# Kernel tuning notes

Hardware: AMD Instinct MI355X
Metric: run time of the kernel (lower is better)

Reference implementation:

```python
import jax, jax.numpy as jnp
import numpy as np

LATENT = 128
DISC = 64
RNN = 512
CODE = 512
INPUT = 2


def _lstm_cell(x, h, c, Wih, Whh, bih, bhh):
    # PyTorch LSTMCell: gate order (i, f, g, o)
    gates = x @ Wih.T + h @ Whh.T + bih + bhh
    i, f, g, o = jnp.split(gates, 4, axis=-1)
    c_new = jax.nn.sigmoid(f) * c + jax.nn.sigmoid(i) * jnp.tanh(g)
    h_new = jax.nn.sigmoid(o) * jnp.tanh(c_new)
    return h_new, c_new


def setup_inputs() -> dict:
    key = jax.random.key(0)
    ks = jax.random.split(key, 12)
    B = 4096
    s = lambda *sh: 1.0 / np.sqrt(sh[-1])
    inp = {
        'latent': jax.random.normal(ks[0], (B, LATENT), dtype=jnp.float32),
        'W_unpack': jax.random.normal(ks[1], (CODE, LATENT + INPUT), dtype=jnp.float32) * s(CODE, LATENT + INPUT),
        'b_unpack': jnp.zeros((CODE,), dtype=jnp.float32),
        'Wih0': jax.random.normal(ks[2], (4 * RNN, CODE), dtype=jnp.float32) * s(4 * RNN, CODE),
        'Whh0': jax.random.normal(ks[3], (4 * RNN, RNN), dtype=jnp.float32) * s(4 * RNN, RNN),
        'bih0': jnp.zeros((4 * RNN,), dtype=jnp.float32),
        'bhh0': jnp.zeros((4 * RNN,), dtype=jnp.float32),
        'Wih1': jax.random.normal(ks[4], (4 * RNN, RNN), dtype=jnp.float32) * s(4 * RNN, RNN),
        'Whh1': jax.random.normal(ks[5], (4 * RNN, RNN), dtype=jnp.float32) * s(4 * RNN, RNN),
        'bih1': jnp.zeros((4 * RNN,), dtype=jnp.float32),
        'bhh1': jnp.zeros((4 * RNN,), dtype=jnp.float32),
        'W_angle': jax.random.normal(ks[6], (DISC, RNN), dtype=jnp.float32) * s(DISC, RNN),
        'b_angle': jnp.zeros((DISC,), dtype=jnp.float32),
        'num_segments': 64,
    }
    return inp


def reference(latent, W_unpack, b_unpack, Wih0, Whh0, bih0, bhh0,
              Wih1, Whh1, bih1, bhh1, W_angle, b_angle, num_segments):
    B = latent.shape[0]
    space = jnp.linspace(-1.0, 1.0, DISC, dtype=latent.dtype)  # [DISC]
    # fixed gumbel noise for all steps: [S, B, DISC]
    u = jax.random.uniform(jax.random.key(42), (num_segments, B, DISC),
                           dtype=latent.dtype, minval=1e-8, maxval=1.0)
    gumbels = -jnp.log(-jnp.log(u))

    def step(carry, g):
        prev, h0, c0, h1, c1 = carry
        x = jnp.tanh(jnp.concatenate([latent, prev], axis=-1) @ W_unpack.T + b_unpack)
        h0, c0 = _lstm_cell(x, h0, c0, Wih0, Whh0, bih0, bhh0)
        h1, c1 = _lstm_cell(h0, h1, c1, Wih1, Whh1, bih1, bhh1)
        logits = h1 @ W_angle.T + b_angle
        # gumbel-softmax, tau=1 (torch default), hard=True with straight-through
        y_soft = jax.nn.softmax(logits + g, axis=-1)
        y_hard = jax.nn.one_hot(jnp.argmax(y_soft, axis=-1), DISC, dtype=y_soft.dtype)
        y = y_soft + jax.lax.stop_gradient(y_hard - y_soft)
        angles = jnp.sum(y * space, axis=-1, keepdims=True)  # [B,1]
        seg = jnp.concatenate([angles, jnp.zeros_like(angles)], axis=-1)  # [B,2]
        return (seg, h0, c0, h1, c1), seg

    z = jnp.zeros((B, RNN), dtype=latent.dtype)
    init = (jnp.zeros((B, INPUT), dtype=latent.dtype), z, z, z, z)
    _, segs = jax.lax.scan(step, init, gumbels)  # [S, B, 2]
    return jnp.transpose(segs, (1, 0, 2))  # [B, S, 2]
```

## Files before the change

kernel.cpp:

```cpp
#include <hip/hip_runtime.h>
#include <cstdint>

#define BATCH 4096
#define LATENT 128
#define RNN 512
#define CODE 512
#define DISC 64
#define NSEG 64
#define UNPACK_COLS 130

__device__ __forceinline__ uint32_t rotl32(uint32_t x, uint32_t r) {
  return (x << r) | (x >> (32u - r));
}

__device__ __forceinline__ uint32_t threefry_bits(uint32_t n) {
  const uint32_t k0 = 0u, k1 = 42u;
  const uint32_t ks2 = k0 ^ k1 ^ 0x1BD11BDAu;
  uint32_t x0 = 0u, x1 = n;
  x0 += k0; x1 += k1;
#define TF_ROUND(r) { x0 += x1; x1 = rotl32(x1, r); x1 ^= x0; }
  TF_ROUND(13) TF_ROUND(15) TF_ROUND(26) TF_ROUND(6)
  x0 += k1;  x1 += ks2 + 1u;
  TF_ROUND(17) TF_ROUND(29) TF_ROUND(16) TF_ROUND(24)
  x0 += ks2; x1 += k0 + 2u;
  TF_ROUND(13) TF_ROUND(15) TF_ROUND(26) TF_ROUND(6)
  x0 += k0;  x1 += k1 + 3u;
  TF_ROUND(17) TF_ROUND(29) TF_ROUND(16) TF_ROUND(24)
  x0 += k1;  x1 += ks2 + 4u;
  TF_ROUND(13) TF_ROUND(15) TF_ROUND(26) TF_ROUND(6)
  x0 += ks2; x1 += k0 + 5u;
#undef TF_ROUND
  return x0 ^ x1;
}

__device__ __forceinline__ float sigmoidf_(float v) {
  return 1.0f / (1.0f + expf(-v));
}

__global__ __launch_bounds__(256) void base_kernel(
    const float* __restrict__ latent, const float* __restrict__ Wu,
    const float* __restrict__ bu, float* __restrict__ base) {
  __shared__ float lrow[LATENT];
  const int b = blockIdx.x;
  if (threadIdx.x < LATENT) lrow[threadIdx.x] = latent[b * LATENT + threadIdx.x];
  __syncthreads();
  for (int n = threadIdx.x; n < CODE; n += 256) {
    const float* wr = Wu + (size_t)n * UNPACK_COLS;
    float acc = 0.f;
#pragma unroll 8
    for (int k = 0; k < LATENT; ++k) acc += lrow[k] * wr[k];
    base[(size_t)b * CODE + n] = acc + bu[n];
  }
}

__global__ __launch_bounds__(256) void x_kernel(
    const float* __restrict__ base, const float* __restrict__ angle,
    const float* __restrict__ Wu, float* __restrict__ xo) {
  const int idx = blockIdx.x * 256 + threadIdx.x;
  const int b = idx >> 9;
  const int n = idx & 511;
  xo[idx] = tanhf(base[idx] + angle[b] * Wu[(size_t)n * UNPACK_COLS + 128]);
}

#define BM 128
#define BN 128
#define BK 16

__global__ __launch_bounds__(256) void gemm_lstm(
    const float* __restrict__ A1, const float* __restrict__ W1,
    const float* __restrict__ A2, const float* __restrict__ W2,
    const float* __restrict__ b1, const float* __restrict__ b2,
    float* __restrict__ c_io, float* __restrict__ h_out) {
  const int K = RNN;
  __shared__ __align__(16) float As[BK][BM];
  __shared__ __align__(16) float Ws[BK][BN];
  const int tid = threadIdx.x;
  const int tx = tid & 15, ty = tid >> 4;
  const int bx = blockIdx.x;
  const int rowBase = blockIdx.y * BM;
  const int lrow = tid >> 2;
  const int lk = (tid & 3) * 4;
  const int swz = (tid & 3) << 3;

  float acc[8][8];
#pragma unroll
  for (int i = 0; i < 8; ++i)
#pragma unroll
    for (int j = 0; j < 8; ++j) acc[i][j] = 0.f;

  for (int seg = 0; seg < 2; ++seg) {
    const float* __restrict__ A = seg ? A2 : A1;
    const float* __restrict__ W = seg ? W2 : W1;
    for (int k0 = 0; k0 < K; k0 += BK) {
      __syncthreads();
#pragma unroll
      for (int r = 0; r < 2; ++r) {
        const int rr = lrow + r * 64;
        const int cc = rr ^ swz;
        const float4 va = *(const float4*)&A[(size_t)(rowBase + rr) * K + k0 + lk];
        As[lk + 0][cc] = va.x; As[lk + 1][cc] = va.y;
        As[lk + 2][cc] = va.z; As[lk + 3][cc] = va.w;
        const int wn = ((rr >> 5) * RNN) + (bx << 5) + (rr & 31);
        const float4 vw = *(const float4*)&W[(size_t)wn * K + k0 + lk];
        Ws[lk + 0][cc] = vw.x; Ws[lk + 1][cc] = vw.y;
        Ws[lk + 2][cc] = vw.z; Ws[lk + 3][cc] = vw.w;
      }
      __syncthreads();
#pragma unroll
      for (int kk = 0; kk < BK; ++kk) {
        const int swk = (kk & 12) << 1;
        const float4 a0 = *(const float4*)&As[kk][(ty * 4) ^ swk];
        const float4 a1 = *(const float4*)&As[kk][(64 + ty * 4) ^ swk];
        const float4 w0 = *(const float4*)&Ws[kk][(tx * 4) ^ swk];
        const float4 w1 = *(const float4*)&Ws[kk][(64 + tx * 4) ^ swk];
        const float av[8] = {a0.x, a0.y, a0.z, a0.w, a1.x, a1.y, a1.z, a1.w};
        const float wv[8] = {w0.x, w0.y, w0.z, w0.w, w1.x, w1.y, w1.z, w1.w};
#pragma unroll
        for (int i = 0; i < 8; ++i)
#pragma unroll
          for (int j = 0; j < 8; ++j) acc[i][j] += av[i] * wv[j];
      }
    }
  }

  const int myjl = (tx & 7) * 4;
  const int jbase = (bx << 5) + myjl;
  const int g0 = (tx < 8) ? 0 : 1;
  const int g1 = g0 + 2;
  float bs0[4], bs1[4];
#pragma unroll
  for (int j = 0; j < 4; ++j) {
    bs0[j] = b1[g0 * RNN + jbase + j] + b2[g0 * RNN + jbase + j];
    bs1[j] = b1[g1 * RNN + jbase + j] + b2[g1 * RNN + jbase + j];
  }
  const bool low = (tx < 8);
#pragma unroll
  for (int i = 0; i < 8; ++i) {
    float v0[4], v1[4], p0[4], p1[4];
#pragma unroll
    for (int j = 0; j < 4; ++j) {
      v0[j] = acc[i][j] + bs0[j];
      v1[j] = acc[i][4 + j] + bs1[j];
      p0[j] = __shfl_xor(v0[j], 8);
      p1[j] = __shfl_xor(v1[j], 8);
    }
    const bool mine = low ? (i < 4) : (i >= 4);
    if (mine) {
      const int row = rowBase + (low ? (ty * 4 + i) : (64 + ty * 4 + (i - 4)));
      const size_t off = (size_t)row * RNN + jbase;
      const float4 cold = *(const float4*)&c_io[off];
      const float co[4] = {cold.x, cold.y, cold.z, cold.w};
      float cn[4], hn[4];
#pragma unroll
      for (int j = 0; j < 4; ++j) {
        const float fi = low ? v0[j] : p0[j];
        const float fg = low ? v1[j] : p1[j];
        const float ff = low ? p0[j] : v0[j];
        const float fo = low ? p1[j] : v1[j];
        const float c2 = sigmoidf_(ff) * co[j] + sigmoidf_(fi) * tanhf(fg);
        cn[j] = c2;
        hn[j] = sigmoidf_(fo) * tanhf(c2);
      }
      *(float4*)&c_io[off] = make_float4(cn[0], cn[1], cn[2], cn[3]);
      *(float4*)&h_out[off] = make_float4(hn[0], hn[1], hn[2], hn[3]);
    }
  }
}

__global__ __launch_bounds__(64) void head_kernel(
    const float* __restrict__ h1, const float* __restrict__ Wang,
    const float* __restrict__ bang, float* __restrict__ angle,
    float* __restrict__ out, int s) {
  const int b = blockIdx.x;
  const int d = threadIdx.x;
  const float4* hr = (const float4*)(h1 + (size_t)b * RNN);
  const float4* wr = (const float4*)(Wang + (size_t)d * RNN);
  float acc = 0.f;
#pragma unroll 16
  for (int k = 0; k < RNN / 4; ++k) {
    float4 a = hr[k], w = wr[k];
    acc += a.x * w.x; acc += a.y * w.y; acc += a.z * w.z; acc += a.w * w.w;
  }
  float z = acc + bang[d];
  const uint32_t n = ((uint32_t)s * BATCH + (uint32_t)b) * DISC + (uint32_t)d;
  const uint32_t bits = threefry_bits(n);
  const float f = __uint_as_float((bits >> 9) | 0x3f800000u) - 1.0f;
  const float u = fmaxf(1e-8f, f + 1e-8f);
  const float gum = -logf(-logf(u));
  z += gum;
  float m = z;
#pragma unroll
  for (int off = 32; off; off >>= 1) m = fmaxf(m, __shfl_xor(m, off));
  const float e = expf(z - m);
  float ssum = e;
#pragma unroll
  for (int off = 32; off; off >>= 1) ssum += __shfl_xor(ssum, off);
  const float y = e / ssum;
  float ymax = y;
#pragma unroll
  for (int off = 32; off; off >>= 1) ymax = fmaxf(ymax, __shfl_xor(ymax, off));
  const unsigned long long mask = __ballot(y == ymax);
  const int k = __ffsll(mask) - 1;
  if (d == 0) {
    const float sp = -1.0f + (2.0f / 63.0f) * (float)k;
    angle[b] = sp;
    out[((size_t)b * NSEG + s) * 2 + 0] = sp;
    out[((size_t)b * NSEG + s) * 2 + 1] = 0.0f;
  }
}

extern "C" void kernel_launch(void* const* d_in, const int* in_sizes, int n_in,
                              void* d_out, int out_size, void* d_ws, size_t ws_size,
                              hipStream_t stream) {
  const float* latent   = (const float*)d_in[0];
  const float* W_unpack = (const float*)d_in[1];
  const float* b_unpack = (const float*)d_in[2];
  const float* Wih0     = (const float*)d_in[3];
  const float* Whh0     = (const float*)d_in[4];
  const float* bih0     = (const float*)d_in[5];
  const float* bhh0     = (const float*)d_in[6];
  const float* Wih1     = (const float*)d_in[7];
  const float* Whh1     = (const float*)d_in[8];
  const float* bih1     = (const float*)d_in[9];
  const float* bhh1     = (const float*)d_in[10];
  const float* W_angle  = (const float*)d_in[11];
  const float* b_angle  = (const float*)d_in[12];
  float* out = (float*)d_out;

  const size_t HC = (size_t)BATCH * RNN;
  float* ws    = (float*)d_ws;
  float* h0a   = ws;
  float* h1a   = h0a + HC;
  float* c0    = h1a + HC;
  float* c1    = c0 + HC;
  float* angle = c1 + HC;
  float* h0b   = angle + BATCH;
  float* h1b   = h0b + HC;
  float* x     = h1b + HC;
  float* base  = x + (size_t)BATCH * CODE;

  hipMemsetAsync(ws, 0, (4 * HC + BATCH) * sizeof(float), stream);

  base_kernel<<<BATCH, 256, 0, stream>>>(latent, W_unpack, b_unpack, base);

  dim3 ggrid(16, 32);
  for (int s = 0; s < NSEG; ++s) {
    const int p = s & 1;
    float* h0p = p ? h0b : h0a; float* h0n = p ? h0a : h0b;
    float* h1p = p ? h1b : h1a; float* h1n = p ? h1a : h1b;
    x_kernel<<<(BATCH * CODE) / 256, 256, 0, stream>>>(base, angle, W_unpack, x);
    gemm_lstm<<<ggrid, 256, 0, stream>>>(x, Wih0, h0p, Whh0, bih0, bhh0, c0, h0n);
    gemm_lstm<<<ggrid, 256, 0, stream>>>(h0n, Wih1, h1p, Whh1, bih1, bhh1, c1, h1n);
    head_kernel<<<BATCH, 64, 0, stream>>>(h1n, W_angle, b_angle, angle, out, s);
  }
}
```

Before: 33.79 ms.

## Prefetch GEMM tiles into registers with BK=32 and stage head weights in LDS

The LSTM GEMM now uses a K tile of 32 and keeps the next tile's global loads in flight in registers while the current tile is computed from shared memory. This hides global load latency and halves the number of barrier pairs, with a new XOR swizzle sized for the wider tile. The head kernel now handles 16 batch rows per 256-thread block and loads W_angle once into 128KB of swizzled LDS, instead of each 64-thread block reading the whole matrix from global memory. The costs are higher register pressure in the GEMM and lower occupancy in the head kernel because of the large LDS footprint.

```diff
diff --git a/kernel.cpp b/kernel.cpp
--- a/kernel.cpp
+++ b/kernel.cpp
@@ -64,7 +64,8 @@
 
 #define BM 128
 #define BN 128
-#define BK 16
+#define BK 32
+#define KSTEPS 32
 
 __global__ __launch_bounds__(256) void gemm_lstm(
     const float* __restrict__ A1, const float* __restrict__ W1,
@@ -79,8 +80,8 @@
   const int bx = blockIdx.x;
   const int rowBase = blockIdx.y * BM;
   const int lrow = tid >> 2;
-  const int lk = (tid & 3) * 4;
-  const int swz = (tid & 3) << 3;
+  const int q = tid & 3;
+  const int lk = q * 4;
 
   float acc[8][8];
 #pragma unroll
@@ -88,40 +89,68 @@
 #pragma unroll
     for (int j = 0; j < 8; ++j) acc[i][j] = 0.f;
 
-  for (int seg = 0; seg < 2; ++seg) {
-    const float* __restrict__ A = seg ? A2 : A1;
-    const float* __restrict__ W = seg ? W2 : W1;
-    for (int k0 = 0; k0 < K; k0 += BK) {
-      __syncthreads();
-#pragma unroll
-      for (int r = 0; r < 2; ++r) {
-        const int rr = lrow + r * 64;
-        const int cc = rr ^ swz;
-        const float4 va = *(const float4*)&A[(size_t)(rowBase + rr) * K + k0 + lk];
-        As[lk + 0][cc] = va.x; As[lk + 1][cc] = va.y;
-        As[lk + 2][cc] = va.z; As[lk + 3][cc] = va.w;
-        const int wn = ((rr >> 5) * RNN) + (bx << 5) + (rr & 31);
-        const float4 vw = *(const float4*)&W[(size_t)wn * K + k0 + lk];
-        Ws[lk + 0][cc] = vw.x; Ws[lk + 1][cc] = vw.y;
-        Ws[lk + 2][cc] = vw.z; Ws[lk + 3][cc] = vw.w;
+  float4 ra[2][2], rw[2][2];
+
+  int wn[2];
+#pragma unroll
+  for (int r = 0; r < 2; ++r) {
+    const int rr = lrow + r * 64;
+    wn[r] = ((rr >> 5) * RNN) + (bx << 5) + (rr & 31);
+  }
+
+#define ISSUE_LOADS(step)                                                      \
+  {                                                                            \
+    const int seg_ = (step) >> 4;                                              \
+    const int k0_ = ((step) & 15) * BK;                                        \
+    const float* __restrict__ A_ = seg_ ? A2 : A1;                             \
+    const float* __restrict__ W_ = seg_ ? W2 : W1;                             \
+    _Pragma("unroll") for (int r = 0; r < 2; ++r) {                            \
+      const int rr_ = lrow + r * 64;                                           \
+      _Pragma("unroll") for (int kh = 0; kh < 2; ++kh) {                       \
+        ra[r][kh] = *(const float4*)&A_[(size_t)(rowBase + rr_) * K + k0_ +    \
+                                        kh * 16 + lk];                         \
+        rw[r][kh] = *(const float4*)&W_[(size_t)wn[r] * K + k0_ + kh * 16 +    \
+                                        lk];                                   \
+      }                                                                        \
+    }                                                                          \
+  }
+
+  ISSUE_LOADS(0)
+
+  for (int step = 0; step < KSTEPS; ++step) {
+    __syncthreads();
+#pragma unroll
+    for (int r = 0; r < 2; ++r) {
+      const int rr = lrow + r * 64;
+#pragma unroll
+      for (int kh = 0; kh < 2; ++kh) {
+        const int kq = q + kh * 4;
+        const int cc = rr ^ (kq << 3);
+        const int kb = kh * 16 + lk;
+        As[kb + 0][cc] = ra[r][kh].x; As[kb + 1][cc] = ra[r][kh].y;
+        As[kb + 2][cc] = ra[r][kh].z; As[kb + 3][cc] = ra[r][kh].w;
+        Ws[kb + 0][cc] = rw[r][kh].x; Ws[kb + 1][cc] = rw[r][kh].y;
+        Ws[kb + 2][cc] = rw[r][kh].z; Ws[kb + 3][cc] = rw[r][kh].w;
       }
-      __syncthreads();
-#pragma unroll
-      for (int kk = 0; kk < BK; ++kk) {
-        const int swk = (kk & 12) << 1;
-        const float4 a0 = *(const float4*)&As[kk][(ty * 4) ^ swk];
-        const float4 a1 = *(const float4*)&As[kk][(64 + ty * 4) ^ swk];
-        const float4 w0 = *(const float4*)&Ws[kk][(tx * 4) ^ swk];
-        const float4 w1 = *(const float4*)&Ws[kk][(64 + tx * 4) ^ swk];
-        const float av[8] = {a0.x, a0.y, a0.z, a0.w, a1.x, a1.y, a1.z, a1.w};
-        const float wv[8] = {w0.x, w0.y, w0.z, w0.w, w1.x, w1.y, w1.z, w1.w};
-#pragma unroll
-        for (int i = 0; i < 8; ++i)
-#pragma unroll
-          for (int j = 0; j < 8; ++j) acc[i][j] += av[i] * wv[j];
-      }
-    }
-  }
+    }
+    __syncthreads();
+    if (step + 1 < KSTEPS) ISSUE_LOADS(step + 1)
+#pragma unroll
+    for (int kk = 0; kk < BK; ++kk) {
+      const int swk = ((kk >> 2) & 7) << 3;
+      const float4 a0 = *(const float4*)&As[kk][(ty * 4) ^ swk];
+      const float4 a1 = *(const float4*)&As[kk][(64 + ty * 4) ^ swk];
+      const float4 w0 = *(const float4*)&Ws[kk][(tx * 4) ^ swk];
+      const float4 w1 = *(const float4*)&Ws[kk][(64 + tx * 4) ^ swk];
+      const float av[8] = {a0.x, a0.y, a0.z, a0.w, a1.x, a1.y, a1.z, a1.w};
+      const float wv[8] = {w0.x, w0.y, w0.z, w0.w, w1.x, w1.y, w1.z, w1.w};
+#pragma unroll
+      for (int i = 0; i < 8; ++i)
+#pragma unroll
+        for (int j = 0; j < 8; ++j) acc[i][j] += av[i] * wv[j];
+    }
+  }
+#undef ISSUE_LOADS
 
   const int myjl = (tx & 7) * 4;
   const int jbase = (bx << 5) + myjl;
@@ -167,45 +196,62 @@
   }
 }
 
-__global__ __launch_bounds__(64) void head_kernel(
+#define HROWS 16
+
+__global__ __launch_bounds__(256) void head_kernel(
     const float* __restrict__ h1, const float* __restrict__ Wang,
     const float* __restrict__ bang, float* __restrict__ angle,
     float* __restrict__ out, int s) {
-  const int b = blockIdx.x;
-  const int d = threadIdx.x;
-  const float4* hr = (const float4*)(h1 + (size_t)b * RNN);
-  const float4* wr = (const float4*)(Wang + (size_t)d * RNN);
-  float acc = 0.f;
+  __shared__ __align__(16) float4 Wl[DISC * 128];
+  const int tid = threadIdx.x;
+  for (int u = tid; u < DISC * 128; u += 256) {
+    const int d = u >> 7, k4 = u & 127;
+    Wl[(d << 7) | (k4 ^ (d & 7))] =
+        *(const float4*)&Wang[((size_t)d << 9) + (k4 << 2)];
+  }
+  __syncthreads();
+  const int wave = tid >> 6;
+  const int d = tid & 63;
+  const int dsw = d & 7;
+  const float bd = bang[d];
+  const int rowBase = blockIdx.x * HROWS + wave * 4;
+#pragma unroll 1
+  for (int rr = 0; rr < 4; ++rr) {
+    const int b = rowBase + rr;
+    const float4* __restrict__ hr = (const float4*)(h1 + ((size_t)b << 9));
+    float acc = 0.f;
 #pragma unroll 16
-  for (int k = 0; k < RNN / 4; ++k) {
-    float4 a = hr[k], w = wr[k];
-    acc += a.x * w.x; acc += a.y * w.y; acc += a.z * w.z; acc += a.w * w.w;
-  }
-  float z = acc + bang[d];
-  const uint32_t n = ((uint32_t)s * BATCH + (uint32_t)b) * DISC + (uint32_t)d;
-  const uint32_t bits = threefry_bits(n);
-  const float f = __uint_as_float((bits >> 9) | 0x3f800000u) - 1.0f;
-  const float u = fmaxf(1e-8f, f + 1e-8f);
-  const float gum = -logf(-logf(u));
-  z += gum;
-  float m = z;
-#pragma unroll
-  for (int off = 32; off; off >>= 1) m = fmaxf(m, __shfl_xor(m, off));
-  const float e = expf(z - m);
-  float ssum = e;
-#pragma unroll
-  for (int off = 32; off; off >>= 1) ssum += __shfl_xor(ssum, off);
-  const float y = e / ssum;
-  float ymax = y;
-#pragma unroll
-  for (int off = 32; off; off >>= 1) ymax = fmaxf(ymax, __shfl_xor(ymax, off));
-  const unsigned long long mask = __ballot(y == ymax);
-  const int k = __ffsll(mask) - 1;
-  if (d == 0) {
-    const float sp = -1.0f + (2.0f / 63.0f) * (float)k;
-    angle[b] = sp;
-    out[((size_t)b * NSEG + s) * 2 + 0] = sp;
-    out[((size_t)b * NSEG + s) * 2 + 1] = 0.0f;
+    for (int k4 = 0; k4 < 128; ++k4) {
+      const float4 a = hr[k4];
+      const float4 w = Wl[(d << 7) | (k4 ^ dsw)];
+      acc += a.x * w.x; acc += a.y * w.y; acc += a.z * w.z; acc += a.w * w.w;
+    }
+    float z = acc + bd;
+    const uint32_t n = ((uint32_t)s * BATCH + (uint32_t)b) * DISC + (uint32_t)d;
+    const uint32_t bits = threefry_bits(n);
+    const float f = __uint_as_float((bits >> 9) | 0x3f800000u) - 1.0f;
+    const float u = fmaxf(1e-8f, f + 1e-8f);
+    const float gum = -logf(-logf(u));
+    z += gum;
+    float m = z;
+#pragma unroll
+    for (int off = 32; off; off >>= 1) m = fmaxf(m, __shfl_xor(m, off));
+    const float e = expf(z - m);
+    float ssum = e;
+#pragma unroll
+    for (int off = 32; off; off >>= 1) ssum += __shfl_xor(ssum, off);
+    const float y = e / ssum;
+    float ymax = y;
+#pragma unroll
+    for (int off = 32; off; off >>= 1) ymax = fmaxf(ymax, __shfl_xor(ymax, off));
+    const unsigned long long mask = __ballot(y == ymax);
+    const int k = __ffsll(mask) - 1;
+    if (d == 0) {
+      const float sp = -1.0f + (2.0f / 63.0f) * (float)k;
+      angle[b] = sp;
+      out[((size_t)b * NSEG + s) * 2 + 0] = sp;
+      out[((size_t)b * NSEG + s) * 2 + 1] = 0.0f;
+    }
   }
 }
 
@@ -251,6 +297,6 @@
     x_kernel<<<(BATCH * CODE) / 256, 256, 0, stream>>>(base, angle, W_unpack, x);
     gemm_lstm<<<ggrid, 256, 0, stream>>>(x, Wih0, h0p, Whh0, bih0, bhh0, c0, h0n);
     gemm_lstm<<<ggrid, 256, 0, stream>>>(h0n, Wih1, h1p, Whh1, bih1, bhh1, c1, h1n);
-    head_kernel<<<BATCH, 64, 0, stream>>>(h1n, W_angle, b_angle, angle, out, s);
-  }
-}
+    head_kernel<<<BATCH / HROWS, 256, 0, stream>>>(h1n, W_angle, b_angle, angle, out, s);
+  }
+}
```

After: 45.69 ms. 35.2% more time.

## Restructure LSTM GEMM to 64x512 tiles with register-prefetched weights and direct A loads

Applied to the files above, without the earlier changes.

Replaces the 128x128 shared-memory tiled LSTM gate GEMM with 512-thread blocks that each cover 64 batch rows by 512 gate columns. Only the weight tile is staged in LDS, and the next K-slice is prefetched into registers while the current one is computed. Each wave reads its 8 A rows straight from global memory as float4. The block index is remapped so neighbouring blocks share weight or A tiles. This aims to raise reuse of each weight slice and overlap global loads with FMA work. The cost is heavy reliance on cache for the A-operand loads and higher register pressure under launch_bounds(512,2).

```diff
diff --git a/kernel.cpp b/kernel.cpp
--- a/kernel.cpp
+++ b/kernel.cpp
@@ -62,25 +62,26 @@
   xo[idx] = tanhf(base[idx] + angle[b] * Wu[(size_t)n * UNPACK_COLS + 128]);
 }
 
-#define BM 128
-#define BN 128
-#define BK 16
-
-__global__ __launch_bounds__(256) void gemm_lstm(
+#define BMW 64
+#define KSTEP 16
+
+__global__ __launch_bounds__(512, 2) void gemm_lstm(
     const float* __restrict__ A1, const float* __restrict__ W1,
     const float* __restrict__ A2, const float* __restrict__ W2,
     const float* __restrict__ b1, const float* __restrict__ b2,
     float* __restrict__ c_io, float* __restrict__ h_out) {
-  const int K = RNN;
-  __shared__ __align__(16) float As[BK][BM];
-  __shared__ __align__(16) float Ws[BK][BN];
+  __shared__ __align__(16) float Ws[KSTEP][512];
   const int tid = threadIdx.x;
-  const int tx = tid & 15, ty = tid >> 4;
-  const int bx = blockIdx.x;
-  const int rowBase = blockIdx.y * BM;
-  const int lrow = tid >> 2;
-  const int lk = (tid & 3) * 4;
-  const int swz = (tid & 3) << 3;
+  const int lane = tid & 63;
+  const int wv = tid >> 6;
+  const int d = blockIdx.x;
+  const int bx = (d & 7) >> 1;
+  const int by = ((d >> 3) << 1) | (d & 1);
+  const int rowBase = by * BMW;
+
+  const int wn = ((tid >> 7) * RNN) + (bx << 7) + (tid & 127);
+  const float* __restrict__ wrow1 = W1 + (size_t)wn * RNN;
+  const float* __restrict__ wrow2 = W2 + (size_t)wn * RNN;
 
   float acc[8][8];
 #pragma unroll
@@ -90,73 +91,91 @@
 
   for (int seg = 0; seg < 2; ++seg) {
     const float* __restrict__ A = seg ? A2 : A1;
-    const float* __restrict__ W = seg ? W2 : W1;
-    for (int k0 = 0; k0 < K; k0 += BK) {
+    const float* __restrict__ wrow = seg ? wrow2 : wrow1;
+    float4 st[4];
+#pragma unroll
+    for (int q = 0; q < 4; ++q) st[q] = *(const float4*)&wrow[q * 4];
+
+    for (int k0 = 0; k0 < RNN; k0 += KSTEP) {
       __syncthreads();
 #pragma unroll
-      for (int r = 0; r < 2; ++r) {
-        const int rr = lrow + r * 64;
-        const int cc = rr ^ swz;
-        const float4 va = *(const float4*)&A[(size_t)(rowBase + rr) * K + k0 + lk];
-        As[lk + 0][cc] = va.x; As[lk + 1][cc] = va.y;
-        As[lk + 2][cc] = va.z; As[lk + 3][cc] = va.w;
-        const int wn = ((rr >> 5) * RNN) + (bx << 5) + (rr & 31);
-        const float4 vw = *(const float4*)&W[(size_t)wn * K + k0 + lk];
-        Ws[lk + 0][cc] = vw.x; Ws[lk + 1][cc] = vw.y;
-        Ws[lk + 2][cc] = vw.z; Ws[lk + 3][cc] = vw.w;
+      for (int q = 0; q < 4; ++q) {
+        Ws[q * 4 + 0][tid] = st[q].x;
+        Ws[q * 4 + 1][tid] = st[q].y;
+        Ws[q * 4 + 2][tid] = st[q].z;
+        Ws[q * 4 + 3][tid] = st[q].w;
       }
       __syncthreads();
-#pragma unroll
-      for (int kk = 0; kk < BK; ++kk) {
-        const int swk = (kk & 12) << 1;
-        const float4 a0 = *(const float4*)&As[kk][(ty * 4) ^ swk];
-        const float4 a1 = *(const float4*)&As[kk][(64 + ty * 4) ^ swk];
-        const float4 w0 = *(const float4*)&Ws[kk][(tx * 4) ^ swk];
-        const float4 w1 = *(const float4*)&Ws[kk][(64 + tx * 4) ^ swk];
-        const float av[8] = {a0.x, a0.y, a0.z, a0.w, a1.x, a1.y, a1.z, a1.w};
-        const float wv[8] = {w0.x, w0.y, w0.z, w0.w, w1.x, w1.y, w1.z, w1.w};
+      if (k0 + KSTEP < RNN) {
+#pragma unroll
+        for (int q = 0; q < 4; ++q)
+          st[q] = *(const float4*)&wrow[k0 + KSTEP + q * 4];
+      }
+      const float* __restrict__ abase = A + (size_t)(rowBase + wv * 8) * RNN + k0;
+#pragma unroll
+      for (int c4 = 0; c4 < 4; ++c4) {
+        float4 af[8];
 #pragma unroll
         for (int i = 0; i < 8; ++i)
-#pragma unroll
-          for (int j = 0; j < 8; ++j) acc[i][j] += av[i] * wv[j];
+          af[i] = *(const float4*)&abase[(size_t)i * RNN + c4 * 4];
+        float4 wfA[4], wfB[4];
+#pragma unroll
+        for (int kk = 0; kk < 4; ++kk) {
+          wfA[kk] = *(const float4*)&Ws[c4 * 4 + kk][4 * lane];
+          wfB[kk] = *(const float4*)&Ws[c4 * 4 + kk][256 + 4 * lane];
+        }
+#pragma unroll
+        for (int kk = 0; kk < 4; ++kk) {
+#pragma unroll
+          for (int i = 0; i < 8; ++i) {
+            const float a = ((const float*)&af[i])[kk];
+            acc[i][0] += a * wfA[kk].x;
+            acc[i][1] += a * wfA[kk].y;
+            acc[i][2] += a * wfA[kk].z;
+            acc[i][3] += a * wfA[kk].w;
+            acc[i][4] += a * wfB[kk].x;
+            acc[i][5] += a * wfB[kk].y;
+            acc[i][6] += a * wfB[kk].z;
+            acc[i][7] += a * wfB[kk].w;
+          }
+        }
       }
     }
   }
 
-  const int myjl = (tx & 7) * 4;
-  const int jbase = (bx << 5) + myjl;
-  const int g0 = (tx < 8) ? 0 : 1;
-  const int g1 = g0 + 2;
-  float bs0[4], bs1[4];
+  const int col0 = (bx << 7) + 4 * (lane & 31);
+  const int gA = lane >> 5;
+  const int gB = 2 + gA;
+  float bsA[4], bsB[4];
 #pragma unroll
   for (int j = 0; j < 4; ++j) {
-    bs0[j] = b1[g0 * RNN + jbase + j] + b2[g0 * RNN + jbase + j];
-    bs1[j] = b1[g1 * RNN + jbase + j] + b2[g1 * RNN + jbase + j];
-  }
-  const bool low = (tx < 8);
+    bsA[j] = b1[gA * RNN + col0 + j] + b2[gA * RNN + col0 + j];
+    bsB[j] = b1[gB * RNN + col0 + j] + b2[gB * RNN + col0 + j];
+  }
+  const bool low = (lane < 32);
 #pragma unroll
   for (int i = 0; i < 8; ++i) {
-    float v0[4], v1[4], p0[4], p1[4];
+    float vA[4], vB[4], pA[4], pB[4];
 #pragma unroll
     for (int j = 0; j < 4; ++j) {
-      v0[j] = acc[i][j] + bs0[j];
-      v1[j] = acc[i][4 + j] + bs1[j];
-      p0[j] = __shfl_xor(v0[j], 8);
-      p1[j] = __shfl_xor(v1[j], 8);
+      vA[j] = acc[i][j] + bsA[j];
+      vB[j] = acc[i][4 + j] + bsB[j];
+      pA[j] = __shfl_xor(vA[j], 32);
+      pB[j] = __shfl_xor(vB[j], 32);
     }
     const bool mine = low ? (i < 4) : (i >= 4);
     if (mine) {
-      const int row = rowBase + (low ? (ty * 4 + i) : (64 + ty * 4 + (i - 4)));
-      const size_t off = (size_t)row * RNN + jbase;
+      const int row = rowBase + wv * 8 + i;
+      const size_t off = (size_t)row * RNN + col0;
       const float4 cold = *(const float4*)&c_io[off];
       const float co[4] = {cold.x, cold.y, cold.z, cold.w};
       float cn[4], hn[4];
 #pragma unroll
       for (int j = 0; j < 4; ++j) {
-        const float fi = low ? v0[j] : p0[j];
-        const float fg = low ? v1[j] : p1[j];
-        const float ff = low ? p0[j] : v0[j];
-        const float fo = low ? p1[j] : v1[j];
+        const float fi = low ? vA[j] : pA[j];
+        const float ff = low ? pA[j] : vA[j];
+        const float fg = low ? vB[j] : pB[j];
+        const float fo = low ? pB[j] : vB[j];
         const float c2 = sigmoidf_(ff) * co[j] + sigmoidf_(fi) * tanhf(fg);
         cn[j] = c2;
         hn[j] = sigmoidf_(fo) * tanhf(c2);
@@ -243,14 +262,13 @@
 
   base_kernel<<<BATCH, 256, 0, stream>>>(latent, W_unpack, b_unpack, base);
 
-  dim3 ggrid(16, 32);
   for (int s = 0; s < NSEG; ++s) {
     const int p = s & 1;
     float* h0p = p ? h0b : h0a; float* h0n = p ? h0a : h0b;
     float* h1p = p ? h1b : h1a; float* h1n = p ? h1a : h1b;
     x_kernel<<<(BATCH * CODE) / 256, 256, 0, stream>>>(base, angle, W_unpack, x);
-    gemm_lstm<<<ggrid, 256, 0, stream>>>(x, Wih0, h0p, Whh0, bih0, bhh0, c0, h0n);
-    gemm_lstm<<<ggrid, 256, 0, stream>>>(h0n, Wih1, h1p, Whh1, bih1, bhh1, c1, h1n);
+    gemm_lstm<<<256, 512, 0, stream>>>(x, Wih0, h0p, Whh0, bih0, bhh0, c0, h0n);
+    gemm_lstm<<<256, 512, 0, stream>>>(h0n, Wih1, h1p, Whh1, bih1, bhh1, c1, h1n);
     head_kernel<<<BATCH, 64, 0, stream>>>(h1n, W_angle, b_angle, angle, out, s);
   }
 }
```

Result: slower. 41.67 ms (+23.3%).

## Use 128-thread GEMM blocks with 8x16 register tiles covering all four gates

Applied to the files above, without the earlier changes.

Rewrites the fused LSTM GEMM to run 128 threads per block, each computing an 8x16 accumulator tile that holds all four gates (i,f,g,o) for 4 hidden units. This removes the cross-lane shuffles in the epilogue, and every thread now writes its outputs instead of half of them idling. Each thread loads a whole 16-wide K slice of one A row and one W row into registers and then stores it unswizzled to LDS. The larger register tile raises register pressure and may cause spills or lower occupancy despite launch_bounds(128,2). The unswizzled LDS writes (As[k][tid]) and float4 reads may change bank-conflict behaviour.

```diff
diff --git a/kernel.cpp b/kernel.cpp
--- a/kernel.cpp
+++ b/kernel.cpp
@@ -66,104 +66,93 @@
 #define BN 128
 #define BK 16
 
-__global__ __launch_bounds__(256) void gemm_lstm(
+__global__ __launch_bounds__(128, 2) void gemm_lstm(
     const float* __restrict__ A1, const float* __restrict__ W1,
     const float* __restrict__ A2, const float* __restrict__ W2,
     const float* __restrict__ b1, const float* __restrict__ b2,
     float* __restrict__ c_io, float* __restrict__ h_out) {
-  const int K = RNN;
   __shared__ __align__(16) float As[BK][BM];
   __shared__ __align__(16) float Ws[BK][BN];
   const int tid = threadIdx.x;
-  const int tx = tid & 15, ty = tid >> 4;
+  const int tx = tid & 7;
+  const int ty = tid >> 3;
   const int bx = blockIdx.x;
   const int rowBase = blockIdx.y * BM;
-  const int lrow = tid >> 2;
-  const int lk = (tid & 3) * 4;
-  const int swz = (tid & 3) << 3;
-
-  float acc[8][8];
+  const int wn = ((tid >> 5) * RNN) + (bx << 5) + (tid & 31);
+  const int arow = rowBase + tid;
+
+  float acc[8][16];
 #pragma unroll
   for (int i = 0; i < 8; ++i)
 #pragma unroll
-    for (int j = 0; j < 8; ++j) acc[i][j] = 0.f;
+    for (int j = 0; j < 16; ++j) acc[i][j] = 0.f;
 
   for (int seg = 0; seg < 2; ++seg) {
-    const float* __restrict__ A = seg ? A2 : A1;
-    const float* __restrict__ W = seg ? W2 : W1;
-    for (int k0 = 0; k0 < K; k0 += BK) {
-      __syncthreads();
-#pragma unroll
-      for (int r = 0; r < 2; ++r) {
-        const int rr = lrow + r * 64;
-        const int cc = rr ^ swz;
-        const float4 va = *(const float4*)&A[(size_t)(rowBase + rr) * K + k0 + lk];
-        As[lk + 0][cc] = va.x; As[lk + 1][cc] = va.y;
-        As[lk + 2][cc] = va.z; As[lk + 3][cc] = va.w;
-        const int wn = ((rr >> 5) * RNN) + (bx << 5) + (rr & 31);
-        const float4 vw = *(const float4*)&W[(size_t)wn * K + k0 + lk];
-        Ws[lk + 0][cc] = vw.x; Ws[lk + 1][cc] = vw.y;
-        Ws[lk + 2][cc] = vw.z; Ws[lk + 3][cc] = vw.w;
+    const float* __restrict__ arp = (seg ? A2 : A1) + (size_t)arow * RNN;
+    const float* __restrict__ wrp = (seg ? W2 : W1) + (size_t)wn * RNN;
+    for (int k0 = 0; k0 < RNN; k0 += BK) {
+      float sa[BK], sw[BK];
+#pragma unroll
+      for (int q = 0; q < 4; ++q) {
+        *(float4*)&sa[q * 4] = *(const float4*)&arp[k0 + q * 4];
+        *(float4*)&sw[q * 4] = *(const float4*)&wrp[k0 + q * 4];
       }
       __syncthreads();
 #pragma unroll
+      for (int k = 0; k < BK; ++k) {
+        As[k][tid] = sa[k];
+        Ws[k][tid] = sw[k];
+      }
+      __syncthreads();
+#pragma unroll
       for (int kk = 0; kk < BK; ++kk) {
-        const int swk = (kk & 12) << 1;
-        const float4 a0 = *(const float4*)&As[kk][(ty * 4) ^ swk];
-        const float4 a1 = *(const float4*)&As[kk][(64 + ty * 4) ^ swk];
-        const float4 w0 = *(const float4*)&Ws[kk][(tx * 4) ^ swk];
-        const float4 w1 = *(const float4*)&Ws[kk][(64 + tx * 4) ^ swk];
+        const float4 a0 = *(const float4*)&As[kk][ty * 8];
+        const float4 a1 = *(const float4*)&As[kk][ty * 8 + 4];
+        float4 w[4];
+#pragma unroll
+        for (int q = 0; q < 4; ++q)
+          w[q] = *(const float4*)&Ws[kk][q * 32 + tx * 4];
         const float av[8] = {a0.x, a0.y, a0.z, a0.w, a1.x, a1.y, a1.z, a1.w};
-        const float wv[8] = {w0.x, w0.y, w0.z, w0.w, w1.x, w1.y, w1.z, w1.w};
-#pragma unroll
-        for (int i = 0; i < 8; ++i)
-#pragma unroll
-          for (int j = 0; j < 8; ++j) acc[i][j] += av[i] * wv[j];
+#pragma unroll
+        for (int i = 0; i < 8; ++i) {
+#pragma unroll
+          for (int q = 0; q < 4; ++q) {
+            acc[i][q * 4 + 0] += av[i] * w[q].x;
+            acc[i][q * 4 + 1] += av[i] * w[q].y;
+            acc[i][q * 4 + 2] += av[i] * w[q].z;
+            acc[i][q * 4 + 3] += av[i] * w[q].w;
+          }
+        }
       }
     }
   }
 
-  const int myjl = (tx & 7) * 4;
-  const int jbase = (bx << 5) + myjl;
-  const int g0 = (tx < 8) ? 0 : 1;
-  const int g1 = g0 + 2;
-  float bs0[4], bs1[4];
-#pragma unroll
-  for (int j = 0; j < 4; ++j) {
-    bs0[j] = b1[g0 * RNN + jbase + j] + b2[g0 * RNN + jbase + j];
-    bs1[j] = b1[g1 * RNN + jbase + j] + b2[g1 * RNN + jbase + j];
-  }
-  const bool low = (tx < 8);
+  const int col0 = (bx << 5) + tx * 4;
+  float bs[4][4];
+#pragma unroll
+  for (int q = 0; q < 4; ++q)
+#pragma unroll
+    for (int j = 0; j < 4; ++j)
+      bs[q][j] = b1[q * RNN + col0 + j] + b2[q * RNN + col0 + j];
 #pragma unroll
   for (int i = 0; i < 8; ++i) {
-    float v0[4], v1[4], p0[4], p1[4];
+    const int row = rowBase + ty * 8 + i;
+    const size_t off = (size_t)row * RNN + col0;
+    const float4 cold = *(const float4*)&c_io[off];
+    const float co[4] = {cold.x, cold.y, cold.z, cold.w};
+    float cn[4], hn[4];
 #pragma unroll
     for (int j = 0; j < 4; ++j) {
-      v0[j] = acc[i][j] + bs0[j];
-      v1[j] = acc[i][4 + j] + bs1[j];
-      p0[j] = __shfl_xor(v0[j], 8);
-      p1[j] = __shfl_xor(v1[j], 8);
+      const float gi = acc[i][0 + j] + bs[0][j];
+      const float gf = acc[i][4 + j] + bs[1][j];
+      const float gg = acc[i][8 + j] + bs[2][j];
+      const float go = acc[i][12 + j] + bs[3][j];
+      const float c2 = sigmoidf_(gf) * co[j] + sigmoidf_(gi) * tanhf(gg);
+      cn[j] = c2;
+      hn[j] = sigmoidf_(go) * tanhf(c2);
     }
-    const bool mine = low ? (i < 4) : (i >= 4);
-    if (mine) {
-      const int row = rowBase + (low ? (ty * 4 + i) : (64 + ty * 4 + (i - 4)));
-      const size_t off = (size_t)row * RNN + jbase;
-      const float4 cold = *(const float4*)&c_io[off];
-      const float co[4] = {cold.x, cold.y, cold.z, cold.w};
-      float cn[4], hn[4];
-#pragma unroll
-      for (int j = 0; j < 4; ++j) {
-        const float fi = low ? v0[j] : p0[j];
-        const float fg = low ? v1[j] : p1[j];
-        const float ff = low ? p0[j] : v0[j];
-        const float fo = low ? p1[j] : v1[j];
-        const float c2 = sigmoidf_(ff) * co[j] + sigmoidf_(fi) * tanhf(fg);
-        cn[j] = c2;
-        hn[j] = sigmoidf_(fo) * tanhf(c2);
-      }
-      *(float4*)&c_io[off] = make_float4(cn[0], cn[1], cn[2], cn[3]);
-      *(float4*)&h_out[off] = make_float4(hn[0], hn[1], hn[2], hn[3]);
-    }
+    *(float4*)&c_io[off] = make_float4(cn[0], cn[1], cn[2], cn[3]);
+    *(float4*)&h_out[off] = make_float4(hn[0], hn[1], hn[2], hn[3]);
   }
 }
 
@@ -249,8 +238,8 @@
     float* h0p = p ? h0b : h0a; float* h0n = p ? h0a : h0b;
     float* h1p = p ? h1b : h1a; float* h1n = p ? h1a : h1b;
     x_kernel<<<(BATCH * CODE) / 256, 256, 0, stream>>>(base, angle, W_unpack, x);
-    gemm_lstm<<<ggrid, 256, 0, stream>>>(x, Wih0, h0p, Whh0, bih0, bhh0, c0, h0n);
-    gemm_lstm<<<ggrid, 256, 0, stream>>>(h0n, Wih1, h1p, Whh1, bih1, bhh1, c1, h1n);
+    gemm_lstm<<<ggrid, 128, 0, stream>>>(x, Wih0, h0p, Whh0, bih0, bhh0, c0, h0n);
+    gemm_lstm<<<ggrid, 128, 0, stream>>>(h0n, Wih1, h1p, Whh1, bih1, bhh1, c1, h1n);
     head_kernel<<<BATCH, 64, 0, stream>>>(h1n, W_angle, b_angle, angle, out, s);
   }
 }
```

Measured after the change: 77.16 ms. 128% more time.
